# Optimization experiments

Hardware: AMD Instinct MI355X
Metric: run time of the kernel (lower is better)

Reference implementation:

```python
import jax, jax.numpy as jnp
import numpy as np

B, F, D = 1024, 256, 64  # batch, featureNumb, featureDim


def setup_inputs() -> dict:
    key = jax.random.key(0)
    k1, k2, k3, k4 = jax.random.split(key, 4)
    feature = jax.random.normal(k1, (B, F, D), dtype=jnp.float32)
    indicator = jax.random.normal(k2, (F, D), dtype=jnp.float32)
    # QKVTransformV2(n, D, D): n stacked DxD linear maps of the indicator
    W_qk = jax.random.normal(k3, (2, D, D), dtype=jnp.float32) / np.float32(np.sqrt(D))
    W_qkv = jax.random.normal(k4, (3, D, D), dtype=jnp.float32) / np.float32(np.sqrt(D))
    return {"feature": feature, "indicator": indicator, "W_qk": W_qk, "W_qkv": W_qkv}


def reference(feature, indicator, W_qk, W_qkv):
    d = indicator.shape[-1]
    scale = jnp.asarray(1.0 / np.sqrt(d), feature.dtype)

    # --- gate branch: QKTrans + DotWeight + LTE (straight-through hard threshold) ---
    trans = jnp.einsum('fd,nde->nfe', indicator, W_qk)            # [2,F,D]
    gate_logits = jnp.einsum('id,jd->ij', trans[0], trans[1]) * scale  # [F,F]
    gate = (gate_logits > 0).astype(feature.dtype)                # LTE forward: hard 0/1 gate

    # --- QKV branch, fused form of the rank-1 outer products ---
    # Original: QKV_outer[t,i,j] = qkv[t,i] (x) qkv[t,j]  (DxD rank-1)
    #           input[b,t,i,j,:] = feature[b,i] @ QKV_outer[t,i,j]
    #                            = (feature[b,i] . qkv[t,i]) * qkv[t,j]
    qkv = jnp.einsum('fd,nde->nfe', indicator, W_qkv)             # [3,F,D]
    s = jnp.einsum('bfd,nfd->nbf', feature, qkv)                  # s[t,b,i] = feature[b,i].qkv[t,i]

    # score[b,i,j] = input[b,0,i,j,:] . input[b,1,j,i,:]
    #              = s[0,b,i] * s[1,b,j] * (qkv[1,i] . qkv[0,j])
    cross = jnp.einsum('id,jd->ij', qkv[1], qkv[0])               # [F,F]
    score = s[0][:, :, None] * s[1][:, None, :] * cross[None]     # [B,F,F]
    scoreHat = score * gate[None]                                 # [B,F,F]

    # output[b,i,:] = sum_j scoreHat[b,i,j] * value[b,i,j,:]
    #               = s[2,b,i] * sum_j scoreHat[b,i,j] * qkv[2,j,:]
    out = s[2][:, :, None] * jnp.einsum('bij,jd->bid', scoreHat, qkv[2])  # [B,F,D]
    return out
```

## Files before the change

### kernel.cpp

```cpp
#include <hip/hip_runtime.h>
#include <stdint.h>

#define B 1024
#define F 256
#define D 64

typedef __attribute__((ext_vector_type(8))) short short8;
typedef __attribute__((ext_vector_type(4))) float f32x4;

__device__ __forceinline__ short f2bf(float f) {
    unsigned u = __builtin_bit_cast(unsigned, f);
    u += 0x7fff + ((u >> 16) & 1);
    return (short)(u >> 16);
}
__device__ __forceinline__ float bf2f(short s) {
    unsigned u = ((unsigned)(unsigned short)s) << 16;
    return __builtin_bit_cast(float, u);
}
__device__ __forceinline__ unsigned pk_bf16(float a, float b) {
    unsigned ua = __builtin_bit_cast(unsigned, a) + 0x8000u;
    unsigned ub = __builtin_bit_cast(unsigned, b) + 0x8000u;
    return __builtin_amdgcn_perm(ub, ua, 0x07060302u);
}


__global__ void precompute_trans(const float* __restrict__ indicator,
                                 const float* __restrict__ W_qk,
                                 const float* __restrict__ W_qkv,
                                 float* __restrict__ trans,
                                 float* __restrict__ qkv) {
    int idx = blockIdx.x * blockDim.x + threadIdx.x;
    int n   = idx / (F * D);
    int rem = idx - n * (F * D);
    int f   = rem / D;
    int e   = rem - f * D;
    const float* W = (n < 2) ? (W_qk + n * D * D) : (W_qkv + (n - 2) * D * D);
    const float* ind = indicator + f * D;
    float acc = 0.f;
#pragma unroll 8
    for (int d = 0; d < D; ++d) acc += ind[d] * W[d * D + e];
    if (n < 2) trans[n * F * D + f * D + e] = acc;
    else       qkv[(n - 2) * F * D + f * D + e] = acc;
}

__global__ __launch_bounds__(256) void s_and_Mt(const float* __restrict__ feature,
                                                const float* __restrict__ trans,
                                                const float* __restrict__ qkv,
                                                float* __restrict__ gS,
                                                short* __restrict__ s1S,
                                                short* __restrict__ At,
                                                short* __restrict__ q2K) {
    int blk = blockIdx.x;
    if (blk < B / 2) {
        int b0 = blk * 2;
        int rg = threadIdx.x >> 4;
        int l  = threadIdx.x & 15;
#pragma unroll 4
        for (int p = 0; p < 16; ++p) {
            int f = p * 16 + rg;
            float4 fv0 = ((const float4*)(feature + ((size_t)(b0 * F + f)) * D))[l];
            float4 fv1 = ((const float4*)(feature + ((size_t)((b0 + 1) * F + f)) * D))[l];
            float4 q0 = ((const float4*)(qkv + f * D))[l];
            float4 q1 = ((const float4*)(qkv + F * D + f * D))[l];
            float4 q2 = ((const float4*)(qkv + 2 * F * D + f * D))[l];
            float a00 = fv0.x * q0.x + fv0.y * q0.y + fv0.z * q0.z + fv0.w * q0.w;
            float a01 = fv0.x * q1.x + fv0.y * q1.y + fv0.z * q1.z + fv0.w * q1.w;
            float a02 = fv0.x * q2.x + fv0.y * q2.y + fv0.z * q2.z + fv0.w * q2.w;
            float a10 = fv1.x * q0.x + fv1.y * q0.y + fv1.z * q0.z + fv1.w * q0.w;
            float a11 = fv1.x * q1.x + fv1.y * q1.y + fv1.z * q1.z + fv1.w * q1.w;
            float a12 = fv1.x * q2.x + fv1.y * q2.y + fv1.z * q2.z + fv1.w * q2.w;
#pragma unroll
            for (int m = 1; m < 16; m <<= 1) {
                a00 += __shfl_xor(a00, m, 64);
                a01 += __shfl_xor(a01, m, 64);
                a02 += __shfl_xor(a02, m, 64);
                a10 += __shfl_xor(a10, m, 64);
                a11 += __shfl_xor(a11, m, 64);
                a12 += __shfl_xor(a12, m, 64);
            }
            if (l == 0) {
                gS[b0 * F + f]        = a00 * a02;
                gS[(b0 + 1) * F + f]  = a10 * a12;
                s1S[b0 * F + f]       = f2bf(a01);
                s1S[(b0 + 1) * F + f] = f2bf(a11);
            }
        }
    } else {
        int j = blk - B / 2;
        int i = threadIdx.x;
        const float4* t0 = (const float4*)(trans + i * D);
        const float4* t1 = (const float4*)(trans + F * D + j * D);
        const float4* q1 = (const float4*)(qkv + F * D + i * D);
        const float4* q0 = (const float4*)(qkv + j * D);
        float d0 = 0.f, d1 = 0.f;
#pragma unroll
        for (int k = 0; k < D / 4; ++k) {
            float4 a = t0[k], b = t1[k], c = q1[k], e = q0[k];
            d0 += a.x * b.x + a.y * b.y + a.z * b.z + a.w * b.w;
            d1 += c.x * e.x + c.y * e.y + c.z * e.z + c.w * e.w;
        }
        float v = (d0 > 0.f) ? d1 : 0.f;
        At[((j >> 5) * F + i) * 32 + (j & 31)] = f2bf(v);
        if (j < D) {
            int p = (j & 3) * 16 + (j >> 2);
            q2K[((i >> 5) * D + p) * 32 + (i & 31)] = f2bf(qkv[2 * F * D + i * D + j]);
        }
    }
}

__global__ __launch_bounds__(512, 4) void gemm_out(const short* __restrict__ At,
                                                   const short* __restrict__ q2K,
                                                   const float* __restrict__ gS,
                                                   const short* __restrict__ s1S,
                                                   float* __restrict__ out) {
    int it  = blockIdx.x & 3;
    int bg  = blockIdx.x >> 2;
    int tid = threadIdx.x;

    __shared__ __align__(16) short AtL[8 * 64 * 32];
    __shared__ __align__(16) short q2L[8 * 64 * 32];

    {
        const float4* Ag = (const float4*)At;
        const float4* Qg = (const float4*)q2K;
        float4* Al = (float4*)AtL;
        float4* Ql = (float4*)q2L;
#pragma unroll
        for (int v = tid; v < 2048; v += 512) {
            int jt = v >> 8, k = v & 255;
            Al[v] = Ag[jt * 1024 + it * 256 + k];
        }
#pragma unroll
        for (int v = tid; v < 2048; v += 512) Ql[v] = Qg[v];
    }
    __syncthreads();

    int w    = tid >> 6;
    int lane = tid & 63;
    int l16  = lane & 15;
    int lq   = lane >> 4;
    int kq   = lq * 8;
    int b    = bg * 8 + w;

    const short* s1b = s1S + b * F;

    f32x4 acc[4][4];
#pragma unroll
    for (int mt = 0; mt < 4; ++mt)
#pragma unroll
        for (int nt = 0; nt < 4; ++nt) acc[mt][nt] = (f32x4){0.f, 0.f, 0.f, 0.f};

    for (int jt = 0; jt < F / 32; ++jt) {
        short8 sv = *(const short8*)(s1b + jt * 32 + kq);
        float sf[8];
#pragma unroll
        for (int e = 0; e < 8; ++e) sf[e] = bf2f(sv[e]);

        short8 bfr[4];
#pragma unroll
        for (int nt = 0; nt < 4; ++nt) {
            int d = nt * 16 + l16;
            short8 qv = *(const short8*)(q2L + (jt * 64 + d) * 32 + kq);
            int4 packed;
            packed.x = pk_bf16(bf2f(qv[0]) * sf[0], bf2f(qv[1]) * sf[1]);
            packed.y = pk_bf16(bf2f(qv[2]) * sf[2], bf2f(qv[3]) * sf[3]);
            packed.z = pk_bf16(bf2f(qv[4]) * sf[4], bf2f(qv[5]) * sf[5]);
            packed.w = pk_bf16(bf2f(qv[6]) * sf[6], bf2f(qv[7]) * sf[7]);
            bfr[nt] = __builtin_bit_cast(short8, packed);
        }
#pragma unroll
        for (int mt = 0; mt < 4; ++mt) {
            short8 af = *(const short8*)(AtL + (jt * 64 + mt * 16 + l16) * 32 + kq);
#pragma unroll
            for (int nt = 0; nt < 4; ++nt)
                acc[mt][nt] = __builtin_amdgcn_mfma_f32_16x16x32_bf16(
                    af, bfr[nt], acc[mt][nt], 0, 0, 0);
        }
    }

    const float4* g4 = (const float4*)(gS + b * F + it * 64);
#pragma unroll
    for (int mt = 0; mt < 4; ++mt) {
        float4 gg = g4[mt * 4 + lq];
        float* obase = out + ((size_t)(b * F + it * 64 + mt * 16 + lq * 4)) * D + l16 * 4;
        float4 v0 = {gg.x * acc[mt][0][0], gg.x * acc[mt][1][0],
                     gg.x * acc[mt][2][0], gg.x * acc[mt][3][0]};
        float4 v1 = {gg.y * acc[mt][0][1], gg.y * acc[mt][1][1],
                     gg.y * acc[mt][2][1], gg.y * acc[mt][3][1]};
        float4 v2 = {gg.z * acc[mt][0][2], gg.z * acc[mt][1][2],
                     gg.z * acc[mt][2][2], gg.z * acc[mt][3][2]};
        float4 v3 = {gg.w * acc[mt][0][3], gg.w * acc[mt][1][3],
                     gg.w * acc[mt][2][3], gg.w * acc[mt][3][3]};
        *(float4*)(obase + 0 * D) = v0;
        *(float4*)(obase + 1 * D) = v1;
        *(float4*)(obase + 2 * D) = v2;
        *(float4*)(obase + 3 * D) = v3;
    }
}

extern "C" void kernel_launch(void* const* d_in, const int* in_sizes, int n_in,
                              void* d_out, int out_size, void* d_ws, size_t ws_size,
                              hipStream_t stream) {
    const float* feature   = (const float*)d_in[0];
    const float* indicator = (const float*)d_in[1];
    const float* W_qk      = (const float*)d_in[2];
    const float* W_qkv     = (const float*)d_in[3];
    float* out = (float*)d_out;

    float* ws    = (float*)d_ws;
    float* trans = ws;
    float* qkv   = trans + 2 * F * D;
    float* gS    = qkv + 3 * F * D;
    short* At    = (short*)(gS + B * F);
    short* q2K   = At + F * F;
    short* s1S   = q2K + (F / 32) * D * 32;

    hipLaunchKernelGGL(precompute_trans, dim3((5 * F * D) / 256), dim3(256), 0,
                       stream, indicator, W_qk, W_qkv, trans, qkv);
    hipLaunchKernelGGL(s_and_Mt, dim3(B / 2 + F), dim3(256), 0, stream,
                       feature, trans, qkv, gS, s1S, At, q2K);
    hipLaunchKernelGGL(gemm_out, dim3((B / 8) * 4), dim3(512), 0, stream,
                       At, q2K, gS, s1S, out);
}
```

Before: 142.7 us.

## Switch intermediate operands to fp16 and restructure s-reduction thread mapping

Replaces the bf16 intermediates (At, q2K, s1S) with fp16, so the per-tile B-fragment scaling becomes a native packed half multiply instead of manual bf16 unpack, multiply and repack, and the matrix core uses the f16 MFMA. The s_and_Mt kernel moves to 512-thread blocks: each row is reduced by 4 lanes over 4 float4 chunks instead of 16 lanes with a 4-step shuffle, and each gate block now handles two j columns. The risk is fp16 range overflow for the s1 and A values, and coarser reads per thread in the feature pass.

```diff
diff --git a/kernel.cpp b/kernel.cpp
--- a/kernel.cpp
+++ b/kernel.cpp
@@ -5,23 +5,8 @@
 #define F 256
 #define D 64
 
-typedef __attribute__((ext_vector_type(8))) short short8;
+typedef __attribute__((ext_vector_type(8))) _Float16 half8;
 typedef __attribute__((ext_vector_type(4))) float f32x4;
-
-__device__ __forceinline__ short f2bf(float f) {
-    unsigned u = __builtin_bit_cast(unsigned, f);
-    u += 0x7fff + ((u >> 16) & 1);
-    return (short)(u >> 16);
-}
-__device__ __forceinline__ float bf2f(short s) {
-    unsigned u = ((unsigned)(unsigned short)s) << 16;
-    return __builtin_bit_cast(float, u);
-}
-__device__ __forceinline__ unsigned pk_bf16(float a, float b) {
-    unsigned ua = __builtin_bit_cast(unsigned, a) + 0x8000u;
-    unsigned ub = __builtin_bit_cast(unsigned, b) + 0x8000u;
-    return __builtin_amdgcn_perm(ub, ua, 0x07060302u);
-}
 
 
 __global__ void precompute_trans(const float* __restrict__ indicator,
@@ -43,34 +28,42 @@
     else       qkv[(n - 2) * F * D + f * D + e] = acc;
 }
 
-__global__ __launch_bounds__(256) void s_and_Mt(const float* __restrict__ feature,
+__global__ __launch_bounds__(512) void s_and_Mt(const float* __restrict__ feature,
                                                 const float* __restrict__ trans,
                                                 const float* __restrict__ qkv,
                                                 float* __restrict__ gS,
-                                                short* __restrict__ s1S,
-                                                short* __restrict__ At,
-                                                short* __restrict__ q2K) {
+                                                _Float16* __restrict__ s1S,
+                                                _Float16* __restrict__ At,
+                                                _Float16* __restrict__ q2K) {
     int blk = blockIdx.x;
+    int tid = threadIdx.x;
     if (blk < B / 2) {
         int b0 = blk * 2;
-        int rg = threadIdx.x >> 4;
-        int l  = threadIdx.x & 15;
-#pragma unroll 4
-        for (int p = 0; p < 16; ++p) {
-            int f = p * 16 + rg;
-            float4 fv0 = ((const float4*)(feature + ((size_t)(b0 * F + f)) * D))[l];
-            float4 fv1 = ((const float4*)(feature + ((size_t)((b0 + 1) * F + f)) * D))[l];
-            float4 q0 = ((const float4*)(qkv + f * D))[l];
-            float4 q1 = ((const float4*)(qkv + F * D + f * D))[l];
-            float4 q2 = ((const float4*)(qkv + 2 * F * D + f * D))[l];
-            float a00 = fv0.x * q0.x + fv0.y * q0.y + fv0.z * q0.z + fv0.w * q0.w;
-            float a01 = fv0.x * q1.x + fv0.y * q1.y + fv0.z * q1.z + fv0.w * q1.w;
-            float a02 = fv0.x * q2.x + fv0.y * q2.y + fv0.z * q2.z + fv0.w * q2.w;
-            float a10 = fv1.x * q0.x + fv1.y * q0.y + fv1.z * q0.z + fv1.w * q0.w;
-            float a11 = fv1.x * q1.x + fv1.y * q1.y + fv1.z * q1.z + fv1.w * q1.w;
-            float a12 = fv1.x * q2.x + fv1.y * q2.y + fv1.z * q2.z + fv1.w * q2.w;
-#pragma unroll
-            for (int m = 1; m < 16; m <<= 1) {
+        int rg = tid >> 2;
+        int l  = tid & 3;
+#pragma unroll
+        for (int p = 0; p < 2; ++p) {
+            int f = p * 128 + rg;
+            const float4* fp0 = (const float4*)(feature + ((size_t)(b0 * F + f)) * D);
+            const float4* fp1 = (const float4*)(feature + ((size_t)((b0 + 1) * F + f)) * D);
+            const float4* qp0 = (const float4*)(qkv + f * D);
+            const float4* qp1 = (const float4*)(qkv + F * D + f * D);
+            const float4* qp2 = (const float4*)(qkv + 2 * F * D + f * D);
+            float a00 = 0.f, a01 = 0.f, a02 = 0.f, a10 = 0.f, a11 = 0.f, a12 = 0.f;
+#pragma unroll
+            for (int t = 0; t < 4; ++t) {
+                int k = l + 4 * t;
+                float4 fv0 = fp0[k], fv1 = fp1[k];
+                float4 q0 = qp0[k], q1 = qp1[k], q2 = qp2[k];
+                a00 += fv0.x * q0.x + fv0.y * q0.y + fv0.z * q0.z + fv0.w * q0.w;
+                a01 += fv0.x * q1.x + fv0.y * q1.y + fv0.z * q1.z + fv0.w * q1.w;
+                a02 += fv0.x * q2.x + fv0.y * q2.y + fv0.z * q2.z + fv0.w * q2.w;
+                a10 += fv1.x * q0.x + fv1.y * q0.y + fv1.z * q0.z + fv1.w * q0.w;
+                a11 += fv1.x * q1.x + fv1.y * q1.y + fv1.z * q1.z + fv1.w * q1.w;
+                a12 += fv1.x * q2.x + fv1.y * q2.y + fv1.z * q2.z + fv1.w * q2.w;
+            }
+#pragma unroll
+            for (int m = 1; m < 4; m <<= 1) {
                 a00 += __shfl_xor(a00, m, 64);
                 a01 += __shfl_xor(a01, m, 64);
                 a02 += __shfl_xor(a02, m, 64);
@@ -81,13 +74,13 @@
             if (l == 0) {
                 gS[b0 * F + f]        = a00 * a02;
                 gS[(b0 + 1) * F + f]  = a10 * a12;
-                s1S[b0 * F + f]       = f2bf(a01);
-                s1S[(b0 + 1) * F + f] = f2bf(a11);
+                s1S[b0 * F + f]       = (_Float16)a01;
+                s1S[(b0 + 1) * F + f] = (_Float16)a11;
             }
         }
     } else {
-        int j = blk - B / 2;
-        int i = threadIdx.x;
+        int j = (blk - B / 2) * 2 + (tid >> 8);
+        int i = tid & 255;
         const float4* t0 = (const float4*)(trans + i * D);
         const float4* t1 = (const float4*)(trans + F * D + j * D);
         const float4* q1 = (const float4*)(qkv + F * D + i * D);
@@ -100,25 +93,25 @@
             d1 += c.x * e.x + c.y * e.y + c.z * e.z + c.w * e.w;
         }
         float v = (d0 > 0.f) ? d1 : 0.f;
-        At[((j >> 5) * F + i) * 32 + (j & 31)] = f2bf(v);
+        At[((j >> 5) * F + i) * 32 + (j & 31)] = (_Float16)v;
         if (j < D) {
             int p = (j & 3) * 16 + (j >> 2);
-            q2K[((i >> 5) * D + p) * 32 + (i & 31)] = f2bf(qkv[2 * F * D + i * D + j]);
-        }
-    }
-}
-
-__global__ __launch_bounds__(512, 4) void gemm_out(const short* __restrict__ At,
-                                                   const short* __restrict__ q2K,
+            q2K[((i >> 5) * D + p) * 32 + (i & 31)] = (_Float16)qkv[2 * F * D + i * D + j];
+        }
+    }
+}
+
+__global__ __launch_bounds__(512, 4) void gemm_out(const _Float16* __restrict__ At,
+                                                   const _Float16* __restrict__ q2K,
                                                    const float* __restrict__ gS,
-                                                   const short* __restrict__ s1S,
+                                                   const _Float16* __restrict__ s1S,
                                                    float* __restrict__ out) {
     int it  = blockIdx.x & 3;
     int bg  = blockIdx.x >> 2;
     int tid = threadIdx.x;
 
-    __shared__ __align__(16) short AtL[8 * 64 * 32];
-    __shared__ __align__(16) short q2L[8 * 64 * 32];
+    __shared__ __align__(16) _Float16 AtL[8 * 64 * 32];
+    __shared__ __align__(16) _Float16 q2L[8 * 64 * 32];
 
     {
         const float4* Ag = (const float4*)At;
@@ -142,7 +135,7 @@
     int kq   = lq * 8;
     int b    = bg * 8 + w;
 
-    const short* s1b = s1S + b * F;
+    const _Float16* s1b = s1S + b * F;
 
     f32x4 acc[4][4];
 #pragma unroll
@@ -151,29 +144,21 @@
         for (int nt = 0; nt < 4; ++nt) acc[mt][nt] = (f32x4){0.f, 0.f, 0.f, 0.f};
 
     for (int jt = 0; jt < F / 32; ++jt) {
-        short8 sv = *(const short8*)(s1b + jt * 32 + kq);
-        float sf[8];
-#pragma unroll
-        for (int e = 0; e < 8; ++e) sf[e] = bf2f(sv[e]);
-
-        short8 bfr[4];
+        half8 sv = *(const half8*)(s1b + jt * 32 + kq);
+
+        half8 bfr[4];
 #pragma unroll
         for (int nt = 0; nt < 4; ++nt) {
             int d = nt * 16 + l16;
-            short8 qv = *(const short8*)(q2L + (jt * 64 + d) * 32 + kq);
-            int4 packed;
-            packed.x = pk_bf16(bf2f(qv[0]) * sf[0], bf2f(qv[1]) * sf[1]);
-            packed.y = pk_bf16(bf2f(qv[2]) * sf[2], bf2f(qv[3]) * sf[3]);
-            packed.z = pk_bf16(bf2f(qv[4]) * sf[4], bf2f(qv[5]) * sf[5]);
-            packed.w = pk_bf16(bf2f(qv[6]) * sf[6], bf2f(qv[7]) * sf[7]);
-            bfr[nt] = __builtin_bit_cast(short8, packed);
+            half8 qv = *(const half8*)(q2L + (jt * 64 + d) * 32 + kq);
+            bfr[nt] = qv * sv;
         }
 #pragma unroll
         for (int mt = 0; mt < 4; ++mt) {
-            short8 af = *(const short8*)(AtL + (jt * 64 + mt * 16 + l16) * 32 + kq);
+            half8 af = *(const half8*)(AtL + (jt * 64 + mt * 16 + l16) * 32 + kq);
 #pragma unroll
             for (int nt = 0; nt < 4; ++nt)
-                acc[mt][nt] = __builtin_amdgcn_mfma_f32_16x16x32_bf16(
+                acc[mt][nt] = __builtin_amdgcn_mfma_f32_16x16x32_f16(
                     af, bfr[nt], acc[mt][nt], 0, 0, 0);
         }
     }
@@ -211,13 +196,13 @@
     float* trans = ws;
     float* qkv   = trans + 2 * F * D;
     float* gS    = qkv + 3 * F * D;
-    short* At    = (short*)(gS + B * F);
-    short* q2K   = At + F * F;
-    short* s1S   = q2K + (F / 32) * D * 32;
+    _Float16* At  = (_Float16*)(gS + B * F);
+    _Float16* q2K = At + F * F;
+    _Float16* s1S = q2K + (F / 32) * D * 32;
 
     hipLaunchKernelGGL(precompute_trans, dim3((5 * F * D) / 256), dim3(256), 0,
                        stream, indicator, W_qk, W_qkv, trans, qkv);
-    hipLaunchKernelGGL(s_and_Mt, dim3(B / 2 + F), dim3(256), 0, stream,
+    hipLaunchKernelGGL(s_and_Mt, dim3(B / 2 + F / 2), dim3(512), 0, stream,
                        feature, trans, qkv, gS, s1S, At, q2K);
     hipLaunchKernelGGL(gemm_out, dim3((B / 8) * 4), dim3(512), 0, stream,
                        At, q2K, gS, s1S, out);
```

New measurement: 151.2 us. 6.0% more time.
